# Performance work log

Hardware: AMD Instinct MI355X
Metric: run time of the kernel (lower is better)

The kernel has to match this reference:

```python
import jax, jax.numpy as jnp
import numpy as np

N = 16384      # total points
B = 8          # point clouds in batch
PER = N // B   # points per cloud (batch ids sorted in blocks)
M = 4096       # sampled centers (ratio 0.25, strided sampler -> batch-aligned)
K = 64         # max_num_neighbors
R = 0.25       # ball-query radius
C_IN = 128
HID = 256
C_OUT = 256


def setup_inputs() -> dict:
    key = jax.random.key(0)
    k1, k2, k3, k4, k5 = jax.random.split(key, 5)
    x = jax.random.normal(k1, (N, C_IN), dtype=jnp.float32)
    pos = jax.random.uniform(k2, (N, 3), dtype=jnp.float32)  # unit cube
    batch = jnp.repeat(jnp.arange(B, dtype=jnp.int32), PER)  # sorted block batch ids
    lframes = jax.random.normal(k3, (N, 3, 3), dtype=jnp.float32)
    W1 = jax.random.normal(k4, (2 * C_IN + 3, HID), dtype=jnp.float32) * 0.05
    b1 = jnp.zeros((HID,), dtype=jnp.float32)
    W2 = jax.random.normal(k5, (HID, C_OUT), dtype=jnp.float32) * 0.05
    b2 = jnp.zeros((C_OUT,), dtype=jnp.float32)
    return {"x": x, "pos": pos, "batch": batch, "lframes": lframes,
            "W1": W1, "b1": b1, "W2": W2, "b2": b2}


def _ball_query(pos, batch, idx):
    """radius(pos, pos[idx], R, batch, batch[idx], max_num_neighbors=K).
    Returns fixed-size neighbor indices [M, K] + validity mask [M, K]."""
    pos_c = pos[idx]                                  # [M, 3]
    # squared distances via gemm trick (avoid [M, N, 3] broadcast)
    d2 = ((pos_c ** 2).sum(-1)[:, None]
          + (pos ** 2).sum(-1)[None, :]
          - 2.0 * pos_c @ pos.T)                      # [M, N]
    valid = (d2 <= R * R) & (batch[idx][:, None] == batch[None, :])
    score = jnp.where(valid, -d2, -jnp.inf)
    vals, nbr = jax.lax.top_k(score, K)               # K nearest within ball
    return nbr, jnp.isfinite(vals)


def reference(x, pos, batch, lframes, W1, b1, W2, b2):
    # center sampler: strided subsample (batch-aligned since batch is block-sorted)
    idx = jnp.arange(0, N, N // M)                    # [M]
    nbr, vmask = _ball_query(pos, batch, idx)         # [M, K]

    pos_dst = pos[idx]                                # [M, 3]
    x_dst = x[idx]                                    # [M, C_IN]
    lframes_dst = lframes[idx]                        # [M, 3, 3]

    # EdgeConv: per-edge message MLP([x_src, x_dst, lframe_dst @ (pos_src - pos_dst)])
    rel = pos[nbr] - pos_dst[:, None, :]              # [M, K, 3]
    rel_loc = jnp.einsum('mij,mkj->mki', lframes_dst, rel)  # rotate into dst frame
    feats = jnp.concatenate([
        x[nbr],                                        # [M, K, C_IN]
        jnp.broadcast_to(x_dst[:, None, :], (M, K, C_IN)),
        rel_loc,
    ], axis=-1)                                        # [M, K, 2*C_IN+3]

    h = jax.nn.relu(feats @ W1 + b1)                   # [M, K, HID]
    msg = h @ W2 + b2                                  # [M, K, C_OUT]

    # masked max aggregation over valid neighbors
    msg = jnp.where(vmask[..., None], msg, -jnp.inf)
    out = msg.max(axis=1)                              # [M, C_OUT]
    out = jnp.where(jnp.isfinite(out), out, 0.0)
    return out, pos_dst, batch[idx], lframes_dst
```

## Files before the change

### kernel.cpp

```cpp
#include <hip/hip_runtime.h>
#include <hip/hip_bf16.h>

#define N_PTS 16384
#define PER   2048
#define M_CTR 4096
#define KNB   64
#define C_IN  128
#define HID   256
#define C_OUT 256

typedef unsigned short u16;
typedef unsigned int u32;
typedef __attribute__((ext_vector_type(8))) short s8v;
typedef __attribute__((ext_vector_type(4))) float f4v;
typedef __attribute__((ext_vector_type(4))) unsigned int u4v;

static __device__ __forceinline__ float bf2f(u16 u) {
    union { unsigned int i; float f; } v; v.i = ((unsigned int)u) << 16; return v.f;
}
static __device__ __forceinline__ u16 f2bf(float f) {
    union { float f; unsigned int i; } v; v.f = f;
    unsigned int r = v.i + 0x7FFFu + ((v.i >> 16) & 1u);
    return (u16)(r >> 16);
}

__global__ __launch_bounds__(256) void ballq_kernel(
        const float* __restrict__ pos, int* __restrict__ nbr, int* __restrict__ cnt,
        const float* __restrict__ W1, const float* __restrict__ W2,
        u16* __restrict__ W1aT, u16* __restrict__ W1bT, u16* __restrict__ W2T) {
    __shared__ float cd2[1024];
    __shared__ int   cidx[1024];
    __shared__ int   s_n;
    int m = blockIdx.x, tid = threadIdx.x;

    if (m < 256) {
        int gid = m * 256 + tid;
        int cc = gid >> 8, k = gid & 255;
        W2T[gid] = f2bf(W2[k * 256 + cc]);
        if (gid < 32768) {
            int c1 = gid >> 7, k1 = gid & 127;
            W1aT[gid] = f2bf(W1[k1 * 256 + c1]);
            W1bT[gid] = f2bf(W1[(k1 + 128) * 256 + c1]);
        }
    }

    int c = m * 4;
    int base = (m >> 9) << 11;
    if (tid == 0) s_n = 0;
    __syncthreads();
    float cx = pos[c * 3 + 0], cy = pos[c * 3 + 1], cz = pos[c * 3 + 2];
    float A = __fadd_rn(__fadd_rn(__fmul_rn(cx, cx), __fmul_rn(cy, cy)), __fmul_rn(cz, cz));
    float c2x = __fmul_rn(2.0f, cx);
    float c2y = __fmul_rn(2.0f, cy);
    float c2z = __fmul_rn(2.0f, cz);
    for (int s = 0; s < 8; ++s) {
        int j = base + tid + (s << 8);
        float px = pos[j * 3 + 0], py = pos[j * 3 + 1], pz = pos[j * 3 + 2];
        float B = __fadd_rn(__fadd_rn(__fmul_rn(px, px), __fmul_rn(py, py)), __fmul_rn(pz, pz));
        float C = __fmaf_rn(c2z, pz, __fmaf_rn(c2y, py, __fmul_rn(c2x, px)));
        float d2 = __fsub_rn(__fadd_rn(A, B), C);
        if (d2 <= 0.0625f) {
            int a = atomicAdd(&s_n, 1);
            if (a < 1024) { cd2[a] = d2; cidx[a] = j; }
        }
    }
    __syncthreads();
    int V = s_n < 1024 ? s_n : 1024;
    if (V <= KNB) {
        if (tid < KNB) nbr[m * KNB + tid] = (tid < V) ? cidx[tid] : c;
        if (tid == 0) cnt[m] = V;
    } else {
        for (int e = tid; e < V; e += 256) {
            float de = cd2[e]; int ie = cidx[e];
            int rank = 0;
            for (int q = 0; q < V; ++q) {
                float dq = cd2[q];
                rank += (dq < de) || (dq == de && cidx[q] < ie);
            }
            if (rank < KNB) nbr[m * KNB + rank] = cidx[e];
        }
        if (tid == 0) cnt[m] = KNB;
    }
}

__global__ __launch_bounds__(256) void gemm_xw_kernel(
        const float* __restrict__ x, const u16* __restrict__ W1aT, const u16* __restrict__ W1bT,
        const float* __restrict__ b1, u16* __restrict__ u_out, float* __restrict__ v_out) {
    __shared__ u16 x_lds[64 * 136];
    int blk = blockIdx.x, tid = threadIdx.x;
    int mode = blk >= 256 ? 1 : 0;
    int bb = mode ? blk - 256 : blk;
    const u16* WT = mode ? W1bT : W1aT;
    {
        int r = tid >> 2, q = tid & 3;
        int xrow = bb * 64 + r;
        if (mode) xrow *= 4;
        const float* xp = x + xrow * C_IN + q * 32;
        u16* dst = x_lds + r * 136 + q * 32;
        for (int i = 0; i < 8; ++i) {
            f4v f = *(const f4v*)(xp + i * 4);
            dst[i * 4 + 0] = f2bf(f[0]);
            dst[i * 4 + 1] = f2bf(f[1]);
            dst[i * 4 + 2] = f2bf(f[2]);
            dst[i * 4 + 3] = f2bf(f[3]);
        }
    }
    __syncthreads();
    int lane = tid & 63, w = tid >> 6;
    int quad = lane >> 4, l16 = lane & 15;
    int cb = w * 64;
    f4v acc[4][4] = {};
    for (int k0 = 0; k0 < 128; k0 += 32) {
        s8v a[4], b[4];
        for (int rt = 0; rt < 4; ++rt)
            a[rt] = *(const s8v*)&x_lds[(rt * 16 + l16) * 136 + k0 + quad * 8];
        for (int ct = 0; ct < 4; ++ct)
            b[ct] = *(const s8v*)(WT + (cb + ct * 16 + l16) * 128 + k0 + quad * 8);
        for (int rt = 0; rt < 4; ++rt)
            for (int ct = 0; ct < 4; ++ct)
                acc[rt][ct] = __builtin_amdgcn_mfma_f32_16x16x32_bf16(a[rt], b[ct], acc[rt][ct], 0, 0, 0);
    }
    for (int rt = 0; rt < 4; ++rt)
        for (int ct = 0; ct < 4; ++ct)
            for (int g = 0; g < 4; ++g) {
                int row = rt * 16 + quad * 4 + g;
                int col = cb + ct * 16 + l16;
                float val = acc[rt][ct][g];
                int orow = bb * 64 + row;
                if (mode == 0) u_out[orow * 256 + col] = f2bf(val);
                else           v_out[orow * 256 + col] = val + b1[col];
            }
}

__global__ __launch_bounds__(256, 4) void edge_kernel(
        const u16* __restrict__ u, const float* __restrict__ v,
        const u16* __restrict__ W2T, const float* __restrict__ W1,
        const float* __restrict__ b2, const float* __restrict__ pos,
        const float* __restrict__ lframes, const int* __restrict__ batch,
        const int* __restrict__ nbr, const int* __restrict__ cnt,
        float* __restrict__ out0, float* __restrict__ out_pos,
        float* __restrict__ out_batch, float* __restrict__ out_lf) {
    __shared__ u16 h_lds[64 * 264];
    __shared__ f4v relc_lds[64];
    __shared__ int nbr_lds[64];
    __shared__ int s_cnt;

    int blk = blockIdx.x, tid = threadIdx.x;
    int m = ((blk & 7) << 9) | (blk >> 3);
    int c = m * 4;

    if (tid == 0) s_cnt = cnt[m];
    if (tid < 64) {
        int j = nbr[m * KNB + tid];
        nbr_lds[tid] = j;
        float rx = pos[j * 3 + 0] - pos[c * 3 + 0];
        float ry = pos[j * 3 + 1] - pos[c * 3 + 1];
        float rz = pos[j * 3 + 2] - pos[c * 3 + 2];
        const float* lf = lframes + c * 9;
        f4v r;
        r[0] = lf[0] * rx + lf[1] * ry + lf[2] * rz;
        r[1] = lf[3] * rx + lf[4] * ry + lf[5] * rz;
        r[2] = lf[6] * rx + lf[7] * ry + lf[8] * rz;
        r[3] = 0.0f;
        relc_lds[tid] = r;
    }
    if (tid < 3)  out_pos[m * 3 + tid] = pos[c * 3 + tid];
    if (tid == 3) out_batch[m] = (float)batch[c];
    if (tid >= 4 && tid < 13) out_lf[m * 9 + (tid - 4)] = lframes[c * 9 + (tid - 4)];

    int co = (tid & 31) * 8;
    int rs = tid >> 5;
    const float* w1c = W1 + 65536;
    f4v vv0 = *(const f4v*)(v + m * 256 + co);
    f4v vv1 = *(const f4v*)(v + m * 256 + co + 4);
    f4v wa0 = *(const f4v*)(w1c + co),        wa1 = *(const f4v*)(w1c + co + 4);
    f4v wb0 = *(const f4v*)(w1c + 256 + co),  wb1 = *(const f4v*)(w1c + 256 + co + 4);
    f4v wc0 = *(const f4v*)(w1c + 512 + co),  wc1 = *(const f4v*)(w1c + 512 + co + 4);
    __syncthreads();

    #pragma unroll
    for (int ii = 0; ii < 8; ++ii) {
        int k = rs + ii * 8;
        int j = nbr_lds[k];
        f4v r = relc_lds[k];
        u4v uu = *(const u4v*)(u + j * 256 + co);
        float p[8];
        #pragma unroll
        for (int e = 0; e < 8; ++e) {
            u16 ue = (u16)((uu[e >> 1] >> ((e & 1) * 16)) & 0xFFFFu);
            float va = (e < 4) ? vv0[e] : vv1[e - 4];
            float a0 = (e < 4) ? wa0[e] : wa1[e - 4];
            float b0 = (e < 4) ? wb0[e] : wb1[e - 4];
            float c0 = (e < 4) ? wc0[e] : wc1[e - 4];
            float pre = fmaf(r[0], a0, fmaf(r[1], b0, fmaf(r[2], c0, va + bf2f(ue))));
            p[e] = fmaxf(pre, 0.0f);
        }
        u4v pk;
        #pragma unroll
        for (int d = 0; d < 4; ++d)
            pk[d] = __builtin_amdgcn_perm(__float_as_uint(p[2 * d + 1]),
                                          __float_as_uint(p[2 * d]), 0x07060302u);
        *(u4v*)&h_lds[k * 264 + co] = pk;
    }
    __syncthreads();

    int lane = tid & 63, w = tid >> 6;
    int quad = lane >> 4, l16 = lane & 15;
    int cb = w * 64;
    f4v acc[4][4] = {};
    for (int k0 = 0; k0 < 256; k0 += 32) {
        s8v a[4], b[4];
        for (int rt = 0; rt < 4; ++rt)
            a[rt] = *(const s8v*)&h_lds[(rt * 16 + l16) * 264 + k0 + quad * 8];
        for (int ct = 0; ct < 4; ++ct)
            b[ct] = *(const s8v*)(W2T + (cb + ct * 16 + l16) * 256 + k0 + quad * 8);
        for (int rt = 0; rt < 4; ++rt)
            for (int ct = 0; ct < 4; ++ct)
                acc[rt][ct] = __builtin_amdgcn_mfma_f32_16x16x32_bf16(a[rt], b[ct], acc[rt][ct], 0, 0, 0);
    }
    int cv = s_cnt;
    for (int ct = 0; ct < 4; ++ct) {
        float mx = -__builtin_inff();
        for (int rt = 0; rt < 4; ++rt)
            for (int g = 0; g < 4; ++g) {
                int row = rt * 16 + quad * 4 + g;
                float val = acc[rt][ct][g];
                if (row < cv) mx = fmaxf(mx, val);
            }
        mx = fmaxf(mx, __shfl_xor(mx, 16, 64));
        mx = fmaxf(mx, __shfl_xor(mx, 32, 64));
        if (lane < 16) {
            int col = cb + ct * 16 + l16;
            out0[m * 256 + col] = mx + b2[col];
        }
    }
}

extern "C" void kernel_launch(void* const* d_in, const int* in_sizes, int n_in,
                              void* d_out, int out_size, void* d_ws, size_t ws_size,
                              hipStream_t stream) {
    const float* x       = (const float*)d_in[0];
    const float* pos     = (const float*)d_in[1];
    const int*   batch   = (const int*)d_in[2];
    const float* lframes = (const float*)d_in[3];
    const float* W1      = (const float*)d_in[4];
    const float* b1      = (const float*)d_in[5];
    const float* W2      = (const float*)d_in[6];
    const float* b2      = (const float*)d_in[7];

    float* out       = (float*)d_out;
    float* out_pos   = out + M_CTR * 256;
    float* out_batch = out_pos + M_CTR * 3;
    float* out_lf    = out_batch + M_CTR;

    char* ws = (char*)d_ws;
    u16*   u_ws = (u16*)(ws);
    float* v_ws = (float*)(ws + 8388608);
    u16*   W1aT = (u16*)(ws + 12582912);
    u16*   W1bT = (u16*)(ws + 12648448);
    u16*   W2T  = (u16*)(ws + 12713984);
    int*   nbr  = (int*)(ws + 12845056);
    int*   cntp = (int*)(ws + 13893632);

    hipLaunchKernelGGL(ballq_kernel, dim3(M_CTR), dim3(256), 0, stream,
                       pos, nbr, cntp, W1, W2, W1aT, W1bT, W2T);
    hipLaunchKernelGGL(gemm_xw_kernel, dim3(320), dim3(256), 0, stream,
                       x, W1aT, W1bT, b1, u_ws, v_ws);
    hipLaunchKernelGGL(edge_kernel, dim3(M_CTR), dim3(256), 0, stream,
                       u_ws, v_ws, W2T, W1, b2, pos, lframes, batch, nbr, cntp,
                       out, out_pos, out_batch, out_lf);
}
```

Measured before the change: 185.1 us.

## Make edge kernel persistent over 8 centers with double-buffered per-center metadata

The edge kernel now launches 512 blocks of 512 threads. Each block handles 8 centers as four pairs, doing a 128-row MFMA GEMM per pair, and prefetches the next pair's neighbor indices, relative positions, v rows and counts into a second LDS buffer while the current pair is processed. W1 position weights and b2 are loaded once per block instead of once per center. This cuts launch and per-block setup overhead and lets metadata gathers overlap compute. In exchange there are more barriers per block, larger LDS use, and fewer blocks for occupancy. Neighbor indices are stored as u16, which holds because indices are below 16384.

```diff
diff --git a/kernel.cpp b/kernel.cpp
--- a/kernel.cpp
+++ b/kernel.cpp
@@ -15,9 +15,6 @@
 typedef __attribute__((ext_vector_type(4))) float f4v;
 typedef __attribute__((ext_vector_type(4))) unsigned int u4v;
 
-static __device__ __forceinline__ float bf2f(u16 u) {
-    union { unsigned int i; float f; } v; v.i = ((unsigned int)u) << 16; return v.f;
-}
 static __device__ __forceinline__ u16 f2bf(float f) {
     union { float f; unsigned int i; } v; v.f = f;
     unsigned int r = v.i + 0x7FFFu + ((v.i >> 16) & 1u);
@@ -132,107 +129,152 @@
             }
 }
 
-__global__ __launch_bounds__(256, 4) void edge_kernel(
+__global__ __launch_bounds__(512, 4) void edge_kernel(
         const u16* __restrict__ u, const float* __restrict__ v,
         const u16* __restrict__ W2T, const float* __restrict__ W1,
         const float* __restrict__ b2, const float* __restrict__ pos,
         const float* __restrict__ lframes, const int* __restrict__ batch,
-        const int* __restrict__ nbr, const int* __restrict__ cnt,
+        const int* __restrict__ nbrg, const int* __restrict__ cnt,
         float* __restrict__ out0, float* __restrict__ out_pos,
         float* __restrict__ out_batch, float* __restrict__ out_lf) {
-    __shared__ u16 h_lds[64 * 264];
-    __shared__ f4v relc_lds[64];
-    __shared__ int nbr_lds[64];
-    __shared__ int s_cnt;
+    __shared__ u16   h_lds[128 * 264];
+    __shared__ float v_lds[2][2][256];
+    __shared__ float w1c_lds[768];
+    __shared__ float relc_lds[2][2][64][3];
+    __shared__ u16   nbr_lds[2][2][64];
+    __shared__ int   cnt_lds[2][2];
 
     int blk = blockIdx.x, tid = threadIdx.x;
-    int m = ((blk & 7) << 9) | (blk >> 3);
-    int c = m * 4;
-
-    if (tid == 0) s_cnt = cnt[m];
-    if (tid < 64) {
-        int j = nbr[m * KNB + tid];
-        nbr_lds[tid] = j;
-        float rx = pos[j * 3 + 0] - pos[c * 3 + 0];
-        float ry = pos[j * 3 + 1] - pos[c * 3 + 1];
-        float rz = pos[j * 3 + 2] - pos[c * 3 + 2];
-        const float* lf = lframes + c * 9;
-        f4v r;
-        r[0] = lf[0] * rx + lf[1] * ry + lf[2] * rz;
-        r[1] = lf[3] * rx + lf[4] * ry + lf[5] * rz;
-        r[2] = lf[6] * rx + lf[7] * ry + lf[8] * rz;
-        r[3] = 0.0f;
-        relc_lds[tid] = r;
-    }
-    if (tid < 3)  out_pos[m * 3 + tid] = pos[c * 3 + tid];
-    if (tid == 3) out_batch[m] = (float)batch[c];
-    if (tid >= 4 && tid < 13) out_lf[m * 9 + (tid - 4)] = lframes[c * 9 + (tid - 4)];
+    int m0 = ((blk & 7) << 9) | ((blk >> 3) << 3);
+
+    for (int i = tid; i < 768; i += 512) w1c_lds[i] = W1[65536 + i];
+    if (tid < 128) {
+        int g = tid >> 6, t = tid & 63;
+        int mm = m0 + g, cc = mm * 4;
+        int j = nbrg[mm * KNB + t];
+        nbr_lds[0][g][t] = (u16)j;
+        float rx = pos[j * 3 + 0] - pos[cc * 3 + 0];
+        float ry = pos[j * 3 + 1] - pos[cc * 3 + 1];
+        float rz = pos[j * 3 + 2] - pos[cc * 3 + 2];
+        const float* lf = lframes + cc * 9;
+        relc_lds[0][g][t][0] = lf[0] * rx + lf[1] * ry + lf[2] * rz;
+        relc_lds[0][g][t][1] = lf[3] * rx + lf[4] * ry + lf[5] * rz;
+        relc_lds[0][g][t][2] = lf[6] * rx + lf[7] * ry + lf[8] * rz;
+    }
+    v_lds[0][tid >> 8][tid & 255] = v[(m0 + (tid >> 8)) * 256 + (tid & 255)];
+    if (tid == 508) cnt_lds[0][0] = cnt[m0];
+    if (tid == 509) cnt_lds[0][1] = cnt[m0 + 1];
+    if (tid >= 256 && tid < 384) {
+        int g = (tid - 256) >> 4, t = tid & 15;
+        int mm = m0 + g, cc = mm * 4;
+        if (t < 3)            out_pos[mm * 3 + t] = pos[cc * 3 + t];
+        else if (t == 3)      out_batch[mm] = (float)batch[cc];
+        else if (t < 13)      out_lf[mm * 9 + (t - 4)] = lframes[cc * 9 + (t - 4)];
+    }
+    __syncthreads();
 
     int co = (tid & 31) * 8;
     int rs = tid >> 5;
-    const float* w1c = W1 + 65536;
-    f4v vv0 = *(const f4v*)(v + m * 256 + co);
-    f4v vv1 = *(const f4v*)(v + m * 256 + co + 4);
-    f4v wa0 = *(const f4v*)(w1c + co),        wa1 = *(const f4v*)(w1c + co + 4);
-    f4v wb0 = *(const f4v*)(w1c + 256 + co),  wb1 = *(const f4v*)(w1c + 256 + co + 4);
-    f4v wc0 = *(const f4v*)(w1c + 512 + co),  wc1 = *(const f4v*)(w1c + 512 + co + 4);
-    __syncthreads();
-
+    int lane = tid & 63, w = tid >> 6;
+    int quad = lane >> 4, l16 = lane & 15;
+    int cb = (w & 3) * 64;
+    int rbase = (w >> 2) * 64;
+    float b2c[4];
     #pragma unroll
-    for (int ii = 0; ii < 8; ++ii) {
-        int k = rs + ii * 8;
-        int j = nbr_lds[k];
-        f4v r = relc_lds[k];
-        u4v uu = *(const u4v*)(u + j * 256 + co);
-        float p[8];
+    for (int ct = 0; ct < 4; ++ct) b2c[ct] = b2[cb + ct * 16 + l16];
+
+    for (int p = 0; p < 4; ++p) {
+        int pb = p & 1;
+        float wa[8], wb[8], wc[8], vv[2][8];
         #pragma unroll
         for (int e = 0; e < 8; ++e) {
-            u16 ue = (u16)((uu[e >> 1] >> ((e & 1) * 16)) & 0xFFFFu);
-            float va = (e < 4) ? vv0[e] : vv1[e - 4];
-            float a0 = (e < 4) ? wa0[e] : wa1[e - 4];
-            float b0 = (e < 4) ? wb0[e] : wb1[e - 4];
-            float c0 = (e < 4) ? wc0[e] : wc1[e - 4];
-            float pre = fmaf(r[0], a0, fmaf(r[1], b0, fmaf(r[2], c0, va + bf2f(ue))));
-            p[e] = fmaxf(pre, 0.0f);
-        }
-        u4v pk;
+            wa[e] = w1c_lds[co + e];
+            wb[e] = w1c_lds[256 + co + e];
+            wc[e] = w1c_lds[512 + co + e];
+            vv[0][e] = v_lds[pb][0][co + e];
+            vv[1][e] = v_lds[pb][1][co + e];
+        }
         #pragma unroll
-        for (int d = 0; d < 4; ++d)
-            pk[d] = __builtin_amdgcn_perm(__float_as_uint(p[2 * d + 1]),
-                                          __float_as_uint(p[2 * d]), 0x07060302u);
-        *(u4v*)&h_lds[k * 264 + co] = pk;
-    }
-    __syncthreads();
-
-    int lane = tid & 63, w = tid >> 6;
-    int quad = lane >> 4, l16 = lane & 15;
-    int cb = w * 64;
-    f4v acc[4][4] = {};
-    for (int k0 = 0; k0 < 256; k0 += 32) {
-        s8v a[4], b[4];
-        for (int rt = 0; rt < 4; ++rt)
-            a[rt] = *(const s8v*)&h_lds[(rt * 16 + l16) * 264 + k0 + quad * 8];
-        for (int ct = 0; ct < 4; ++ct)
-            b[ct] = *(const s8v*)(W2T + (cb + ct * 16 + l16) * 256 + k0 + quad * 8);
-        for (int rt = 0; rt < 4; ++rt)
+        for (int ii = 0; ii < 8; ++ii) {
+            int row = rs + ii * 16;
+            int g = ii >> 2;
+            int rl = row & 63;
+            int j = (int)nbr_lds[pb][g][rl];
+            u4v uu = *(const u4v*)(u + j * 256 + co);
+            float r0 = relc_lds[pb][g][rl][0];
+            float r1 = relc_lds[pb][g][rl][1];
+            float r2 = relc_lds[pb][g][rl][2];
+            float p8[8];
+            #pragma unroll
+            for (int e = 0; e < 8; ++e) {
+                u32 bits = (e & 1) ? (uu[e >> 1] & 0xFFFF0000u) : (uu[e >> 1] << 16);
+                float pre = fmaf(r0, wa[e], fmaf(r1, wb[e], fmaf(r2, wc[e],
+                              vv[g][e] + __uint_as_float(bits))));
+                p8[e] = fmaxf(pre, 0.0f);
+            }
+            u4v pk;
+            #pragma unroll
+            for (int d = 0; d < 4; ++d)
+                pk[d] = __builtin_amdgcn_perm(__float_as_uint(p8[2 * d + 1]),
+                                              __float_as_uint(p8[2 * d]), 0x07060302u);
+            *(u4v*)&h_lds[row * 264 + co] = pk;
+        }
+        if (p < 3) {
+            int nb = (p + 1) & 1;
+            int mbase = m0 + (p + 1) * 2;
+            if (tid < 128) {
+                int g = tid >> 6, t = tid & 63;
+                int mm = mbase + g, cc = mm * 4;
+                int j = nbrg[mm * KNB + t];
+                nbr_lds[nb][g][t] = (u16)j;
+                float rx = pos[j * 3 + 0] - pos[cc * 3 + 0];
+                float ry = pos[j * 3 + 1] - pos[cc * 3 + 1];
+                float rz = pos[j * 3 + 2] - pos[cc * 3 + 2];
+                const float* lf = lframes + cc * 9;
+                relc_lds[nb][g][t][0] = lf[0] * rx + lf[1] * ry + lf[2] * rz;
+                relc_lds[nb][g][t][1] = lf[3] * rx + lf[4] * ry + lf[5] * rz;
+                relc_lds[nb][g][t][2] = lf[6] * rx + lf[7] * ry + lf[8] * rz;
+            }
+            v_lds[nb][tid >> 8][tid & 255] = v[(mbase + (tid >> 8)) * 256 + (tid & 255)];
+            if (tid == 508) cnt_lds[nb][0] = cnt[mbase];
+            if (tid == 509) cnt_lds[nb][1] = cnt[mbase + 1];
+        }
+        __syncthreads();
+
+        f4v acc[4][4] = {};
+        for (int k0 = 0; k0 < 256; k0 += 32) {
+            s8v a[4], b[4];
+            #pragma unroll
+            for (int rt = 0; rt < 4; ++rt)
+                a[rt] = *(const s8v*)&h_lds[(rbase + rt * 16 + l16) * 264 + k0 + quad * 8];
+            #pragma unroll
             for (int ct = 0; ct < 4; ++ct)
-                acc[rt][ct] = __builtin_amdgcn_mfma_f32_16x16x32_bf16(a[rt], b[ct], acc[rt][ct], 0, 0, 0);
-    }
-    int cv = s_cnt;
-    for (int ct = 0; ct < 4; ++ct) {
-        float mx = -__builtin_inff();
-        for (int rt = 0; rt < 4; ++rt)
-            for (int g = 0; g < 4; ++g) {
-                int row = rt * 16 + quad * 4 + g;
-                float val = acc[rt][ct][g];
-                if (row < cv) mx = fmaxf(mx, val);
-            }
-        mx = fmaxf(mx, __shfl_xor(mx, 16, 64));
-        mx = fmaxf(mx, __shfl_xor(mx, 32, 64));
-        if (lane < 16) {
-            int col = cb + ct * 16 + l16;
-            out0[m * 256 + col] = mx + b2[col];
-        }
+                b[ct] = *(const s8v*)(W2T + (cb + ct * 16 + l16) * 256 + k0 + quad * 8);
+            #pragma unroll
+            for (int rt = 0; rt < 4; ++rt)
+                #pragma unroll
+                for (int ct = 0; ct < 4; ++ct)
+                    acc[rt][ct] = __builtin_amdgcn_mfma_f32_16x16x32_bf16(a[rt], b[ct], acc[rt][ct], 0, 0, 0);
+        }
+        int cv = cnt_lds[pb][w >> 2];
+        int mout = m0 + p * 2 + (w >> 2);
+        #pragma unroll
+        for (int ct = 0; ct < 4; ++ct) {
+            float mx = -__builtin_inff();
+            #pragma unroll
+            for (int rt = 0; rt < 4; ++rt)
+                #pragma unroll
+                for (int g = 0; g < 4; ++g) {
+                    int row = rt * 16 + quad * 4 + g;
+                    float val = acc[rt][ct][g];
+                    if (row < cv) mx = fmaxf(mx, val);
+                }
+            mx = fmaxf(mx, __shfl_xor(mx, 16, 64));
+            mx = fmaxf(mx, __shfl_xor(mx, 32, 64));
+            if (lane < 16)
+                out0[mout * 256 + cb + ct * 16 + l16] = mx + b2c[ct];
+        }
+        __syncthreads();
     }
 }
 
@@ -266,7 +308,7 @@
                        pos, nbr, cntp, W1, W2, W1aT, W1bT, W2T);
     hipLaunchKernelGGL(gemm_xw_kernel, dim3(320), dim3(256), 0, stream,
                        x, W1aT, W1bT, b1, u_ws, v_ws);
-    hipLaunchKernelGGL(edge_kernel, dim3(M_CTR), dim3(256), 0, stream,
+    hipLaunchKernelGGL(edge_kernel, dim3(512), dim3(512), 0, stream,
                        u_ws, v_ws, W2T, W1, b2, pos, lframes, batch, nbr, cntp,
                        out, out_pos, out_batch, out_lf);
 }
```

Measured after the change: 225.3 us. 21.7% more time.
